# Kernel tuning notes

Hardware: AMD Instinct MI355X
Metric: run time of the kernel (lower is better)

Reference implementation:

```python
import jax, jax.numpy as jnp
import numpy as np
from jax import lax

DENSITY = 985.0
NUM_DIRS = 720  # angular samples for support-function convex hull perimeter


def _compute_mass(tris):
    # tris: [B, F, 3, 3]; signed volume per tet against origin, summed.
    x = tris[..., 0]; y = tris[..., 1]; z = tris[..., 2]  # [B, F, 3]
    vol = (-x[:, :, 2] * y[:, :, 1] * z[:, :, 0]
           + x[:, :, 1] * y[:, :, 2] * z[:, :, 0]
           + x[:, :, 2] * y[:, :, 0] * z[:, :, 1]
           - x[:, :, 0] * y[:, :, 2] * z[:, :, 1]
           - x[:, :, 1] * y[:, :, 0] * z[:, :, 2]
           + x[:, :, 0] * y[:, :, 1] * z[:, :, 2]).sum(axis=1)
    return jnp.abs(vol) / 6.0 * DENSITY


def _bary_point(tris, face_idx, bc):
    # tris [B,F,3,3], bc [3] -> [B,3]
    tri = tris[:, face_idx]                      # [B,3,3]
    return (tri * bc.reshape(1, 3, 1)).sum(axis=1)


def _cross_section(tris, h):
    # Intersect every triangle edge with horizontal plane y=h[b].
    # tris [B,F,3,3], h [B] -> points [B, 3F, 3], valid [B, 3F]
    B = tris.shape[0]
    i = jnp.array([0, 1, 2]); j = jnp.array([1, 2, 0])
    y = tris[..., 1]                              # [B,F,3]
    hh = h[:, None, None]
    yi = y[..., i]; yj = y[..., j]                # [B,F,3]
    valid = (yi - hh) * (yj - hh) < 0.0           # edge crosses the plane
    denom = yj - yi
    safe = jnp.where(jnp.abs(denom) > 1e-12, denom, 1e-12)
    # interpolation weights are treated as constants (torch version computes
    # collision bcs under no_grad / detaches them)
    t = lax.stop_gradient(jnp.clip((hh - yi) / safe, 0.0, 1.0))  # [B,F,3]
    vi = tris[:, :, i, :]; vj = tris[:, :, j, :]  # [B,F,3,3]
    pts = vi + t[..., None] * (vj - vi)           # [B,F,3,3]
    return pts.reshape(B, -1, 3), valid.reshape(B, -1)


def _hull_perimeter(pts2, valid):
    # Convex hull perimeter via rotating support points.
    # pts2 [B,P,2], valid [B,P] -> [B]
    theta = jnp.arange(NUM_DIRS, dtype=pts2.dtype) * (2.0 * np.pi / NUM_DIRS)
    dirs = jnp.stack([jnp.cos(theta), jnp.sin(theta)], axis=-1)  # [K,2]
    proj = jnp.einsum('bpc,kc->bpk', pts2, dirs)                 # [B,P,K]
    proj = jnp.where(valid[:, :, None], proj, -jnp.inf)
    idx = jnp.argmax(proj, axis=1)                               # [B,K]
    extreme = jnp.take_along_axis(pts2, idx[..., None], axis=1)  # [B,K,2]
    seg = extreme - jnp.roll(extreme, -1, axis=1)
    return jnp.sqrt((seg * seg).sum(-1) + 1e-20).sum(axis=1)


def _periphery(tris, face_idx, bcs):
    vertex = _bary_point(tris, face_idx, bcs)    # [B,3]
    pts, valid = _cross_section(tris, vertex[:, 1])
    pts2 = pts[..., ::2]                         # (x, z) plane coordinates
    return _hull_perimeter(pts2, valid)


def setup_inputs() -> dict:
    key = jax.random.key(0)
    ks = jax.random.split(key, 6)
    B, F = 4, 20908
    def bc(k):
        u = jax.random.uniform(k, (3,), dtype=jnp.float32) + 0.1
        return u / u.sum()
    return {
        'triangles': jax.random.normal(ks[0], (B, F, 3, 3), dtype=jnp.float32),
        'head_top_bc': bc(ks[1]),
        'left_heel_bc': bc(ks[2]),
        'chest_bcs': bc(ks[3]),
        'belly_bcs': bc(ks[4]),
        'hips_bcs': bc(ks[5]),
        'head_top_face_idx': 100,
        'left_heel_face_idx': 200,
        'chest_face_index': 5000,
        'belly_face_index': 6000,
        'hips_face_index': 7000,
    }


def reference(triangles, head_top_bc, left_heel_bc, chest_bcs, belly_bcs,
              hips_bcs, head_top_face_idx, left_heel_face_idx,
              chest_face_index, belly_face_index, hips_face_index):
    mass = _compute_mass(triangles)
    head_top = _bary_point(triangles, head_top_face_idx, head_top_bc)
    left_heel = _bary_point(triangles, left_heel_face_idx, left_heel_bc)
    height = jnp.abs(head_top[:, 1] - left_heel[:, 1])
    chest = _periphery(triangles, chest_face_index, chest_bcs)
    waist = _periphery(triangles, belly_face_index, belly_bcs)
    hips = _periphery(triangles, hips_face_index, hips_bcs)
    return jnp.stack([mass, height, chest, waist, hips])  # [5, B]
```

## Files before the change

kernel.cpp:

```cpp
#include <hip/hip_runtime.h>
#include <math.h>

#define NUM_DIRS 720
#define CF 512
#define SCHUNK (3 * CF)
#define NPAIRS 12
#define KC 64
#define NCHMAX 64
#define LDSCAP 4096

__device__ __forceinline__ unsigned int ordf(float f) {
    unsigned int b = __float_as_uint(f);
    return (b & 0x80000000u) ? ~b : (b | 0x80000000u);
}
__device__ __forceinline__ float unordf(unsigned int u) {
    unsigned int b = (u & 0x80000000u) ? (u ^ 0x80000000u) : ~u;
    return __uint_as_float(b);
}

__device__ __forceinline__ float plane_h(const float* __restrict__ tris, int F,
                                         int b, int fidx,
                                         const float* __restrict__ bc) {
    const float* vt = tris + ((size_t)(b * F + fidx)) * 9;
    return fmaf(bc[2], vt[7], fmaf(bc[1], vt[4], bc[0] * vt[1]));
}

__device__ __forceinline__ bool crossing(const float* __restrict__ v, int k,
                                         float h, float& px, float& pz) {
    int j = (k == 2) ? 0 : (k + 1);
    float yi = v[k * 3 + 1], yj = v[j * 3 + 1];
    if (!((yi - h) * (yj - h) < 0.f)) return false;
    float denom = yj - yi;
    float safe = (fabsf(denom) > 1e-12f) ? denom : 1e-12f;
    float tt = fminf(fmaxf((h - yi) / safe, 0.f), 1.f);
    px = v[k * 3 + 0] + tt * (v[j * 3 + 0] - v[k * 3 + 0]);
    pz = v[k * 3 + 2] + tt * (v[j * 3 + 2] - v[k * 3 + 2]);
    return true;
}

__global__ __launch_bounds__(256) void coarse_kernel(
    const float* __restrict__ tris, int F, int NCH,
    const float* __restrict__ bc0, const float* __restrict__ bc1,
    const float* __restrict__ bc2,
    const int* __restrict__ fi0, const int* __restrict__ fi1,
    const int* __restrict__ fi2,
    unsigned int* __restrict__ M_part, float* __restrict__ R2_part,
    float* __restrict__ mass_part) {
    int pair = blockIdx.y, chunk = blockIdx.x;
    int m = pair >> 2, b = pair & 3;
    const float* bc = (m == 0) ? bc0 : ((m == 1) ? bc1 : bc2);
    int fidx = (m == 0) ? fi0[0] : ((m == 1) ? fi1[0] : fi2[0]);
    float h = plane_h(tris, F, b, fidx, bc);

    __shared__ float2 sp[SCHUNK];
    __shared__ unsigned int sM[KC];
    __shared__ int cnt;
    __shared__ float redA[4], redB[4];
    if (threadIdx.x < KC) sM[threadIdx.x] = 0;
    if (threadIdx.x == 0) cnt = 0;
    __syncthreads();

    float r2max = 0.f, msum = 0.f;
    int f0 = chunk * CF, fend = min(f0 + CF, F);
    for (int f = f0 + threadIdx.x; f < fend; f += blockDim.x) {
        const float* t = tris + ((size_t)(b * F + f)) * 9;
        float v[9];
#pragma unroll
        for (int i = 0; i < 9; i++) v[i] = t[i];
        if (m == 0) {
            msum += -v[6] * v[4] * v[2] + v[3] * v[7] * v[2]
                    + v[6] * v[1] * v[5] - v[0] * v[7] * v[5]
                    - v[3] * v[1] * v[8] + v[0] * v[4] * v[8];
        }
#pragma unroll
        for (int k = 0; k < 3; k++) {
            float px, pz;
            if (crossing(v, k, h, px, pz)) {
                int n = atomicAdd(&cnt, 1);
                sp[n] = make_float2(px, pz);
                r2max = fmaxf(r2max, px * px + pz * pz);
            }
        }
    }
    int lane = threadIdx.x & 63, w = threadIdx.x >> 6;
    for (int off = 32; off; off >>= 1)
        r2max = fmaxf(r2max, __shfl_down(r2max, off, 64));
    if (lane == 0) redA[w] = r2max;
    if (m == 0) {
        for (int off = 32; off; off >>= 1) msum += __shfl_down(msum, off, 64);
        if (lane == 0) redB[w] = msum;
    }
    __syncthreads();
    if (threadIdx.x == 0) {
        R2_part[pair * NCH + chunk] =
            fmaxf(fmaxf(redA[0], redA[1]), fmaxf(redA[2], redA[3]));
        if (m == 0)
            mass_part[b * NCH + chunk] = redB[0] + redB[1] + redB[2] + redB[3];
    }

    int n = cnt;
    int d = threadIdx.x & (KC - 1);
    int slice = threadIdx.x >> 6;
    float s, c;
    sincosf((float)d * (float)(6.283185307179586 / KC), &s, &c);
    float mv = -INFINITY;
    for (int i = slice; i < n; i += 4) {
        float2 p = sp[i];
        mv = fmaxf(mv, fmaf(p.x, c, p.y * s));
    }
    atomicMax(&sM[d], ordf(mv));
    __syncthreads();
    if (threadIdx.x < KC)
        M_part[(pair * NCH + chunk) * KC + threadIdx.x] = sM[threadIdx.x];
}

__global__ __launch_bounds__(256) void surv_kernel(
    const float* __restrict__ tris, int F, int NCH,
    const float* __restrict__ bc0, const float* __restrict__ bc1,
    const float* __restrict__ bc2,
    const int* __restrict__ fi0, const int* __restrict__ fi1,
    const int* __restrict__ fi2,
    const unsigned int* __restrict__ M_part,
    const float* __restrict__ R2_part,
    int* __restrict__ cnt_part, float2* __restrict__ slist) {
    int pair = blockIdx.y, chunk = blockIdx.x;
    int m = pair >> 2, b = pair & 3;
    const float* bc = (m == 0) ? bc0 : ((m == 1) ? bc1 : bc2);
    int fidx = (m == 0) ? fi0[0] : ((m == 1) ? fi1[0] : fi2[0]);
    float h = plane_h(tris, F, b, fidx, bc);

    __shared__ float minM_s, rmax_s;
    __shared__ int cnt;
    int tid = threadIdx.x;
    if (tid < 64) {
        unsigned int mx = 0;
        for (int c = 0; c < NCH; c++)
            mx = max(mx, M_part[(pair * NCH + c) * KC + tid]);
        float Md = unordf(mx);
        for (int off = 32; off; off >>= 1)
            Md = fminf(Md, __shfl_down(Md, off, 64));
        if (tid == 0) minM_s = Md;
    } else if (tid < 128) {
        int c = tid - 64;
        float r2 = (c < NCH) ? R2_part[pair * NCH + c] : 0.f;
        for (int off = 32; off; off >>= 1)
            r2 = fmaxf(r2, __shfl_down(r2, off, 64));
        if (tid == 64) rmax_s = r2;
    }
    if (tid == 0) cnt = 0;
    __syncthreads();
    float tau = minM_s - 0.052f * sqrtf(rmax_s);
    bool useTau = (tau > 0.f);
    float tau2 = tau * tau;

    float2* seg = slist + (size_t)(pair * NCH + chunk) * SCHUNK;
    int f0 = chunk * CF, fend = min(f0 + CF, F);
    for (int f = f0 + tid; f < fend; f += blockDim.x) {
        const float* t = tris + ((size_t)(b * F + f)) * 9;
        float v[9];
#pragma unroll
        for (int i = 0; i < 9; i++) v[i] = t[i];
#pragma unroll
        for (int k = 0; k < 3; k++) {
            float px, pz;
            if (crossing(v, k, h, px, pz)) {
                float r2 = px * px + pz * pz;
                if (!useTau || r2 >= tau2) {
                    int idx = atomicAdd(&cnt, 1);
                    seg[idx] = make_float2(px, pz);
                }
            }
        }
    }
    __syncthreads();
    if (tid == 0) cnt_part[pair * NCH + chunk] = cnt;
}

__global__ __launch_bounds__(256) void final_kernel(
    const float* __restrict__ tris, int F, int NCH,
    const float* __restrict__ htbc, const float* __restrict__ lhbc,
    const int* __restrict__ hti, const int* __restrict__ lhi,
    const int* __restrict__ cnt_part, const float2* __restrict__ slist,
    const float* __restrict__ mass_part, float* __restrict__ out) {
    int pair = blockIdx.x;
    int m = pair >> 2, b = pair & 3;
    int tid = threadIdx.x;

    if (pair == 0) {
        if (tid >= 64 && tid < 68) {
            int bb = tid - 64;
            float s = 0.f;
            for (int c = 0; c < NCH; c++) s += mass_part[bb * NCH + c];
            out[bb] = fabsf(s) / 6.0f * 985.0f;
        }
        if (tid >= 96 && tid < 100) {
            int bb = tid - 96;
            float hy = plane_h(tris, F, bb, hti[0], htbc);
            float ly = plane_h(tris, F, bb, lhi[0], lhbc);
            out[4 + bb] = fabsf(hy - ly);
        }
    }

    __shared__ int soff[NCHMAX + 1];
    __shared__ float2 sp[LDSCAP];
    __shared__ float ex[NUM_DIRS], ez[NUM_DIRS];
    __shared__ float wsum[4];

    if (tid == 0) {
        int acc = 0;
        soff[0] = 0;
        for (int c = 0; c < NCH; c++) {
            acc += cnt_part[pair * NCH + c];
            soff[c + 1] = acc;
        }
    }
    __syncthreads();
    int ns = soff[NCH];

    for (int c = 0; c < NCH; c++) {
        int base = soff[c], nc = soff[c + 1] - base;
        const float2* seg = slist + (size_t)(pair * NCH + c) * SCHUNK;
        for (int i = tid; i < nc; i += 256) {
            int g = base + i;
            if (g < LDSCAP) sp[g] = seg[i];
        }
    }
    __syncthreads();

    const float dth = (float)(6.283185307179586 / NUM_DIRS);
    int d0 = tid, d1 = tid + 256, d2 = tid + 512;
    float c0, s0, c1, s1, c2 = 0.f, s2 = 0.f;
    sincosf((float)d0 * dth, &s0, &c0);
    sincosf((float)d1 * dth, &s1, &c1);
    if (d2 < NUM_DIRS) sincosf((float)d2 * dth, &s2, &c2);

    float bp0 = -INFINITY, bp1 = -INFINITY, bp2 = -INFINITY;
    float bx0 = 0.f, bz0 = 0.f, bx1 = 0.f, bz1 = 0.f, bx2 = 0.f, bz2 = 0.f;
    int nl = min(ns, LDSCAP);
    for (int i = 0; i < nl; i++) {
        float2 p = sp[i];
        float q0 = fmaf(p.x, c0, p.y * s0);
        float q1 = fmaf(p.x, c1, p.y * s1);
        float q2 = fmaf(p.x, c2, p.y * s2);
        if (q0 > bp0) { bp0 = q0; bx0 = p.x; bz0 = p.y; }
        if (q1 > bp1) { bp1 = q1; bx1 = p.x; bz1 = p.y; }
        if (q2 > bp2) { bp2 = q2; bx2 = p.x; bz2 = p.y; }
    }
    if (ns > LDSCAP) {
        for (int c = 0; c < NCH; c++) {
            int base = soff[c], e = soff[c + 1];
            const float2* seg = slist + (size_t)(pair * NCH + c) * SCHUNK;
            for (int g = max(base, LDSCAP); g < e; g++) {
                float2 p = seg[g - base];
                float q0 = fmaf(p.x, c0, p.y * s0);
                float q1 = fmaf(p.x, c1, p.y * s1);
                float q2 = fmaf(p.x, c2, p.y * s2);
                if (q0 > bp0) { bp0 = q0; bx0 = p.x; bz0 = p.y; }
                if (q1 > bp1) { bp1 = q1; bx1 = p.x; bz1 = p.y; }
                if (q2 > bp2) { bp2 = q2; bx2 = p.x; bz2 = p.y; }
            }
        }
    }
    ex[d0] = bx0; ez[d0] = bz0;
    ex[d1] = bx1; ez[d1] = bz1;
    if (d2 < NUM_DIRS) { ex[d2] = bx2; ez[d2] = bz2; }
    __syncthreads();

    float local = 0.f;
    for (int d = tid; d < NUM_DIRS; d += 256) {
        int dn = (d + 1) % NUM_DIRS;
        float dx = ex[d] - ex[dn];
        float dz = ez[d] - ez[dn];
        local += sqrtf(dx * dx + dz * dz + 1e-20f);
    }
    int lane = tid & 63, w = tid >> 6;
    for (int off = 32; off; off >>= 1) local += __shfl_down(local, off, 64);
    if (lane == 0) wsum[w] = local;
    __syncthreads();
    if (tid == 0)
        out[(2 + m) * 4 + b] = wsum[0] + wsum[1] + wsum[2] + wsum[3];
}

extern "C" void kernel_launch(void* const* d_in, const int* in_sizes, int n_in,
                              void* d_out, int out_size, void* d_ws,
                              size_t ws_size, hipStream_t stream) {
    const float* tris = (const float*)d_in[0];
    const float* htbc = (const float*)d_in[1];
    const float* lhbc = (const float*)d_in[2];
    const float* cbc  = (const float*)d_in[3];
    const float* bbc  = (const float*)d_in[4];
    const float* hbc  = (const float*)d_in[5];
    const int* hti = (const int*)d_in[6];
    const int* lhi = (const int*)d_in[7];
    const int* cfi = (const int*)d_in[8];
    const int* bfi = (const int*)d_in[9];
    const int* hfi = (const int*)d_in[10];
    float* out = (float*)d_out;

    int F = in_sizes[0] / 36;
    int NCH = (F + CF - 1) / CF;

    char* w = (char*)d_ws;
    size_t off = 0;
    unsigned int* M_part = (unsigned int*)(w + off);
    off += (size_t)NPAIRS * NCH * KC * sizeof(unsigned int);
    float* R2_part = (float*)(w + off);
    off += (size_t)NPAIRS * NCH * sizeof(float);
    int* cnt_part = (int*)(w + off);
    off += (size_t)NPAIRS * NCH * sizeof(int);
    float* mass_part = (float*)(w + off);
    off += (size_t)4 * NCH * sizeof(float);
    off = (off + 255) & ~(size_t)255;
    float2* slist = (float2*)(w + off);

    dim3 g(NCH, NPAIRS);
    coarse_kernel<<<g, 256, 0, stream>>>(tris, F, NCH, cbc, bbc, hbc, cfi,
                                         bfi, hfi, M_part, R2_part, mass_part);
    surv_kernel<<<g, 256, 0, stream>>>(tris, F, NCH, cbc, bbc, hbc, cfi, bfi,
                                       hfi, M_part, R2_part, cnt_part, slist);
    final_kernel<<<NPAIRS, 256, 0, stream>>>(tris, F, NCH, htbc, lhbc, hti,
                                             lhi, cnt_part, slist, mass_part,
                                             out);
}
```

Before: 50.21 us.

## Aggregate LDS atomics per wavefront, double chunk size, parallelize reductions and unroll scans

Replaces per-thread shared atomicAdd appends with wavefront ballot/popcount aggregation in both the coarse and survivor kernels. It doubles the faces per chunk, which halves the block count and the number of partial results. The survivor kernel now reduces the per-chunk maxima across all waves, and the final kernel builds its offsets with a wave prefix scan. The support-point loops are unrolled with independent accumulators. The larger chunks reduce grid parallelism, and the smaller LDS cap makes the global-memory fallback path more likely.

```diff
diff --git a/kernel.cpp b/kernel.cpp
--- a/kernel.cpp
+++ b/kernel.cpp
@@ -2,12 +2,12 @@
 #include <math.h>
 
 #define NUM_DIRS 720
-#define CF 512
+#define CF 1024
 #define SCHUNK (3 * CF)
 #define NPAIRS 12
 #define KC 64
 #define NCHMAX 64
-#define LDSCAP 4096
+#define LDSCAP 3072
 
 __device__ __forceinline__ unsigned int ordf(float f) {
     unsigned int b = __float_as_uint(f);
@@ -51,18 +51,19 @@
     const float* bc = (m == 0) ? bc0 : ((m == 1) ? bc1 : bc2);
     int fidx = (m == 0) ? fi0[0] : ((m == 1) ? fi1[0] : fi2[0]);
     float h = plane_h(tris, F, b, fidx, bc);
+    int tid = threadIdx.x, lane = tid & 63, w = tid >> 6;
 
     __shared__ float2 sp[SCHUNK];
     __shared__ unsigned int sM[KC];
     __shared__ int cnt;
     __shared__ float redA[4], redB[4];
-    if (threadIdx.x < KC) sM[threadIdx.x] = 0;
-    if (threadIdx.x == 0) cnt = 0;
+    if (tid < KC) sM[tid] = 0;
+    if (tid == 0) cnt = 0;
     __syncthreads();
 
     float r2max = 0.f, msum = 0.f;
     int f0 = chunk * CF, fend = min(f0 + CF, F);
-    for (int f = f0 + threadIdx.x; f < fend; f += blockDim.x) {
+    for (int f = f0 + tid; f < fend; f += 256) {
         const float* t = tris + ((size_t)(b * F + f)) * 9;
         float v[9];
 #pragma unroll
@@ -75,14 +76,22 @@
 #pragma unroll
         for (int k = 0; k < 3; k++) {
             float px, pz;
-            if (crossing(v, k, h, px, pz)) {
-                int n = atomicAdd(&cnt, 1);
-                sp[n] = make_float2(px, pz);
-                r2max = fmaxf(r2max, px * px + pz * pz);
+            bool has = crossing(v, k, h, px, pz);
+            unsigned long long mask = __ballot(has);
+            if (mask) {
+                int leader = __ffsll((long long)mask) - 1;
+                int base = 0;
+                if (lane == leader) base = atomicAdd(&cnt, __popcll(mask));
+                base = __shfl(base, leader, 64);
+                if (has) {
+                    int idx =
+                        base + __popcll(mask & ((1ull << lane) - 1ull));
+                    sp[idx] = make_float2(px, pz);
+                    r2max = fmaxf(r2max, px * px + pz * pz);
+                }
             }
         }
     }
-    int lane = threadIdx.x & 63, w = threadIdx.x >> 6;
     for (int off = 32; off; off >>= 1)
         r2max = fmaxf(r2max, __shfl_down(r2max, off, 64));
     if (lane == 0) redA[w] = r2max;
@@ -91,7 +100,7 @@
         if (lane == 0) redB[w] = msum;
     }
     __syncthreads();
-    if (threadIdx.x == 0) {
+    if (tid == 0) {
         R2_part[pair * NCH + chunk] =
             fmaxf(fmaxf(redA[0], redA[1]), fmaxf(redA[2], redA[3]));
         if (m == 0)
@@ -99,19 +108,27 @@
     }
 
     int n = cnt;
-    int d = threadIdx.x & (KC - 1);
-    int slice = threadIdx.x >> 6;
+    int d = lane;
+    int slice = w;
     float s, c;
     sincosf((float)d * (float)(6.283185307179586 / KC), &s, &c);
-    float mv = -INFINITY;
-    for (int i = slice; i < n; i += 4) {
+    float mv0 = -INFINITY, mv1 = -INFINITY, mv2 = -INFINITY, mv3 = -INFINITY;
+    int i = slice;
+    for (; i + 12 < n; i += 16) {
+        float2 pa = sp[i], pb = sp[i + 4], pc = sp[i + 8], pd = sp[i + 12];
+        mv0 = fmaxf(mv0, fmaf(pa.x, c, pa.y * s));
+        mv1 = fmaxf(mv1, fmaf(pb.x, c, pb.y * s));
+        mv2 = fmaxf(mv2, fmaf(pc.x, c, pc.y * s));
+        mv3 = fmaxf(mv3, fmaf(pd.x, c, pd.y * s));
+    }
+    for (; i < n; i += 4) {
         float2 p = sp[i];
-        mv = fmaxf(mv, fmaf(p.x, c, p.y * s));
-    }
+        mv0 = fmaxf(mv0, fmaf(p.x, c, p.y * s));
+    }
+    float mv = fmaxf(fmaxf(mv0, mv1), fmaxf(mv2, mv3));
     atomicMax(&sM[d], ordf(mv));
     __syncthreads();
-    if (threadIdx.x < KC)
-        M_part[(pair * NCH + chunk) * KC + threadIdx.x] = sM[threadIdx.x];
+    if (tid < KC) M_part[(pair * NCH + chunk) * KC + tid] = sM[tid];
 }
 
 __global__ __launch_bounds__(256) void surv_kernel(
@@ -128,34 +145,49 @@
     const float* bc = (m == 0) ? bc0 : ((m == 1) ? bc1 : bc2);
     int fidx = (m == 0) ? fi0[0] : ((m == 1) ? fi1[0] : fi2[0]);
     float h = plane_h(tris, F, b, fidx, bc);
-
-    __shared__ float minM_s, rmax_s;
+    int tid = threadIdx.x, lane = tid & 63, w = tid >> 6;
+
+    __shared__ unsigned int sMd[KC];
+    __shared__ float sR[4];
+    __shared__ float tau_s;
     __shared__ int cnt;
-    int tid = threadIdx.x;
+    if (tid < KC) sMd[tid] = 0;
+    if (tid == 0) cnt = 0;
+    __syncthreads();
+
+    {
+        int d = lane, part = w;
+        unsigned int mx = 0;
+        for (int c2 = part; c2 < NCH; c2 += 4)
+            mx = max(mx, M_part[(pair * NCH + c2) * KC + d]);
+        atomicMax(&sMd[d], mx);
+    }
+    {
+        float r2 = 0.f;
+        for (int c2 = tid; c2 < NCH; c2 += 256)
+            r2 = fmaxf(r2, R2_part[pair * NCH + c2]);
+        for (int off = 32; off; off >>= 1)
+            r2 = fmaxf(r2, __shfl_down(r2, off, 64));
+        if (lane == 0) sR[w] = r2;
+    }
+    __syncthreads();
     if (tid < 64) {
-        unsigned int mx = 0;
-        for (int c = 0; c < NCH; c++)
-            mx = max(mx, M_part[(pair * NCH + c) * KC + tid]);
-        float Md = unordf(mx);
+        float Md = unordf(sMd[tid]);
         for (int off = 32; off; off >>= 1)
             Md = fminf(Md, __shfl_down(Md, off, 64));
-        if (tid == 0) minM_s = Md;
-    } else if (tid < 128) {
-        int c = tid - 64;
-        float r2 = (c < NCH) ? R2_part[pair * NCH + c] : 0.f;
-        for (int off = 32; off; off >>= 1)
-            r2 = fmaxf(r2, __shfl_down(r2, off, 64));
-        if (tid == 64) rmax_s = r2;
-    }
-    if (tid == 0) cnt = 0;
-    __syncthreads();
-    float tau = minM_s - 0.052f * sqrtf(rmax_s);
+        if (tid == 0) {
+            float R = sqrtf(fmaxf(fmaxf(sR[0], sR[1]), fmaxf(sR[2], sR[3])));
+            tau_s = Md - 0.052f * R;
+        }
+    }
+    __syncthreads();
+    float tau = tau_s;
     bool useTau = (tau > 0.f);
     float tau2 = tau * tau;
 
     float2* seg = slist + (size_t)(pair * NCH + chunk) * SCHUNK;
     int f0 = chunk * CF, fend = min(f0 + CF, F);
-    for (int f = f0 + tid; f < fend; f += blockDim.x) {
+    for (int f = f0 + tid; f < fend; f += 256) {
         const float* t = tris + ((size_t)(b * F + f)) * 9;
         float v[9];
 #pragma unroll
@@ -163,10 +195,20 @@
 #pragma unroll
         for (int k = 0; k < 3; k++) {
             float px, pz;
+            bool keep = false;
             if (crossing(v, k, h, px, pz)) {
                 float r2 = px * px + pz * pz;
-                if (!useTau || r2 >= tau2) {
-                    int idx = atomicAdd(&cnt, 1);
+                keep = (!useTau || r2 >= tau2);
+            }
+            unsigned long long mask = __ballot(keep);
+            if (mask) {
+                int leader = __ffsll((long long)mask) - 1;
+                int base = 0;
+                if (lane == leader) base = atomicAdd(&cnt, __popcll(mask));
+                base = __shfl(base, leader, 64);
+                if (keep) {
+                    int idx =
+                        base + __popcll(mask & ((1ull << lane) - 1ull));
                     seg[idx] = make_float2(px, pz);
                 }
             }
@@ -184,7 +226,7 @@
     const float* __restrict__ mass_part, float* __restrict__ out) {
     int pair = blockIdx.x;
     int m = pair >> 2, b = pair & 3;
-    int tid = threadIdx.x;
+    int tid = threadIdx.x, lane = tid & 63, w = tid >> 6;
 
     if (pair == 0) {
         if (tid >= 64 && tid < 68) {
@@ -201,24 +243,28 @@
         }
     }
 
-    __shared__ int soff[NCHMAX + 1];
+    __shared__ int soff[NCHMAX];
+    __shared__ int scnt_s[NCHMAX];
+    __shared__ int ns_s;
     __shared__ float2 sp[LDSCAP];
     __shared__ float ex[NUM_DIRS], ez[NUM_DIRS];
     __shared__ float wsum[4];
 
-    if (tid == 0) {
-        int acc = 0;
-        soff[0] = 0;
-        for (int c = 0; c < NCH; c++) {
-            acc += cnt_part[pair * NCH + c];
-            soff[c + 1] = acc;
-        }
-    }
-    __syncthreads();
-    int ns = soff[NCH];
+    if (tid < 64) {
+        int v = (tid < NCH) ? cnt_part[pair * NCH + tid] : 0;
+        int s = v;
+        for (int off = 1; off < 64; off <<= 1) {
+            int o = __shfl_up(s, off, 64);
+            if (lane >= off) s += o;
+        }
+        if (tid < NCH) { soff[tid] = s - v; scnt_s[tid] = v; }
+        if (tid == 63) ns_s = s;
+    }
+    __syncthreads();
+    int ns = ns_s;
 
     for (int c = 0; c < NCH; c++) {
-        int base = soff[c], nc = soff[c + 1] - base;
+        int base = soff[c], nc = scnt_s[c];
         const float2* seg = slist + (size_t)(pair * NCH + c) * SCHUNK;
         for (int i = tid; i < nc; i += 256) {
             int g = base + i;
@@ -237,7 +283,29 @@
     float bp0 = -INFINITY, bp1 = -INFINITY, bp2 = -INFINITY;
     float bx0 = 0.f, bz0 = 0.f, bx1 = 0.f, bz1 = 0.f, bx2 = 0.f, bz2 = 0.f;
     int nl = min(ns, LDSCAP);
-    for (int i = 0; i < nl; i++) {
+    int i = 0;
+    for (; i + 3 < nl; i += 4) {
+        float2 pa = sp[i], pb = sp[i + 1], pc = sp[i + 2], pd = sp[i + 3];
+        float qa0 = fmaf(pa.x, c0, pa.y * s0), qb0 = fmaf(pb.x, c0, pb.y * s0);
+        float qc0 = fmaf(pc.x, c0, pc.y * s0), qd0 = fmaf(pd.x, c0, pd.y * s0);
+        if (qa0 > bp0) { bp0 = qa0; bx0 = pa.x; bz0 = pa.y; }
+        if (qb0 > bp0) { bp0 = qb0; bx0 = pb.x; bz0 = pb.y; }
+        if (qc0 > bp0) { bp0 = qc0; bx0 = pc.x; bz0 = pc.y; }
+        if (qd0 > bp0) { bp0 = qd0; bx0 = pd.x; bz0 = pd.y; }
+        float qa1 = fmaf(pa.x, c1, pa.y * s1), qb1 = fmaf(pb.x, c1, pb.y * s1);
+        float qc1 = fmaf(pc.x, c1, pc.y * s1), qd1 = fmaf(pd.x, c1, pd.y * s1);
+        if (qa1 > bp1) { bp1 = qa1; bx1 = pa.x; bz1 = pa.y; }
+        if (qb1 > bp1) { bp1 = qb1; bx1 = pb.x; bz1 = pb.y; }
+        if (qc1 > bp1) { bp1 = qc1; bx1 = pc.x; bz1 = pc.y; }
+        if (qd1 > bp1) { bp1 = qd1; bx1 = pd.x; bz1 = pd.y; }
+        float qa2 = fmaf(pa.x, c2, pa.y * s2), qb2 = fmaf(pb.x, c2, pb.y * s2);
+        float qc2 = fmaf(pc.x, c2, pc.y * s2), qd2 = fmaf(pd.x, c2, pd.y * s2);
+        if (qa2 > bp2) { bp2 = qa2; bx2 = pa.x; bz2 = pa.y; }
+        if (qb2 > bp2) { bp2 = qb2; bx2 = pb.x; bz2 = pb.y; }
+        if (qc2 > bp2) { bp2 = qc2; bx2 = pc.x; bz2 = pc.y; }
+        if (qd2 > bp2) { bp2 = qd2; bx2 = pd.x; bz2 = pd.y; }
+    }
+    for (; i < nl; i++) {
         float2 p = sp[i];
         float q0 = fmaf(p.x, c0, p.y * s0);
         float q1 = fmaf(p.x, c1, p.y * s1);
@@ -248,7 +316,7 @@
     }
     if (ns > LDSCAP) {
         for (int c = 0; c < NCH; c++) {
-            int base = soff[c], e = soff[c + 1];
+            int base = soff[c], e = soff[c] + scnt_s[c];
             const float2* seg = slist + (size_t)(pair * NCH + c) * SCHUNK;
             for (int g = max(base, LDSCAP); g < e; g++) {
                 float2 p = seg[g - base];
@@ -273,7 +341,6 @@
         float dz = ez[d] - ez[dn];
         local += sqrtf(dx * dx + dz * dz + 1e-20f);
     }
-    int lane = tid & 63, w = tid >> 6;
     for (int off = 32; off; off >>= 1) local += __shfl_down(local, off, 64);
     if (lane == 0) wsum[w] = local;
     __syncthreads();
```

Result: faster. 42.48 us (-15.4%).
